# Optimization experiments

Hardware: AMD Instinct MI355X
Metric: run time of the kernel (lower is better)

## Reference

```python
import jax, jax.numpy as jnp
import numpy as np

B, N, DIM = 8, 1024, 768
HEADS, HEAD_DIM = 12, 64
INNER = HEADS * HEAD_DIM  # 768
SCALE = HEAD_DIM ** -0.5


def setup_inputs() -> dict:
    key = jax.random.key(0)
    k1, k2, k3, k4 = jax.random.split(key, 4)
    x = jax.random.normal(k1, (B, N, DIM), dtype=jnp.float32)
    # nn.Linear weights, stored as (in, out) for x @ W
    w_qkv = jax.random.normal(k2, (DIM, 3 * INNER), dtype=jnp.float32) * (DIM ** -0.5)
    w_out = jax.random.normal(k3, (INNER, DIM), dtype=jnp.float32) * (INNER ** -0.5)
    b_out = jax.random.normal(k4, (DIM,), dtype=jnp.float32) * 0.02
    return {"x": x, "w_qkv": w_qkv, "w_out": w_out, "b_out": b_out}


def reference(x, w_qkv, w_out, b_out):
    qkv = jnp.einsum('bnd,de->bne', x, w_qkv)  # [B, N, 3*INNER]
    q, k, v = jnp.split(qkv, 3, axis=-1)
    # 'b n (h d) -> b h n d'
    def split_heads(t):
        return t.reshape(B, N, HEADS, HEAD_DIM).transpose(0, 2, 1, 3)
    q, k, v = split_heads(q), split_heads(k), split_heads(v)
    score = jnp.einsum('bhnd,bhmd->bhnm', q, k) * SCALE  # [B, H, N, N]
    # Faithful to torch nn.Softmax() with dim=None on a 4D tensor: legacy
    # behavior applies softmax over dim=1 (the HEADS axis), NOT the key axis.
    attention = jax.nn.softmax(score, axis=1)
    out = jnp.einsum('bhnm,bhmd->bhnd', attention, v)  # [B, H, N, D]
    out = out.transpose(0, 2, 1, 3).reshape(B, N, INNER)  # 'b h n d -> b n (h d)'
    return jnp.einsum('bne,ed->bnd', out, w_out) + b_out
```

## Files before the change

### kernel.cpp

```cpp
#include <hip/hip_runtime.h>

typedef float  f32x4  __attribute__((ext_vector_type(4)));
typedef short  bf16x8 __attribute__((ext_vector_type(8)));

#define MFMA16(a, b, c) __builtin_amdgcn_mfma_f32_16x16x32_bf16((a), (b), (c), 0, 0, 0)

#define GLL16(g, l) __builtin_amdgcn_global_load_lds(                      \
    (const __attribute__((address_space(1))) void*)(g),                    \
    (__attribute__((address_space(3))) void*)(l), 16, 0, 0)

__device__ __forceinline__ short f2bf(float f) {
    union { float f; unsigned u; } a; a.f = f;
    unsigned r = a.u + 0x7fffu + ((a.u >> 16) & 1u);
    return (short)(r >> 16);
}
__device__ __forceinline__ float bf2f(unsigned short u) {
    union { unsigned u; float f; } a; a.u = ((unsigned)u) << 16; return a.f;
}

#define Bb   8
#define Nn   1024
#define DIM  768
#define HH   12
#define HD   64
#define INNER 768
#define SCALE 0.125f
#define SCL2E 0.18033688011112042f

__global__ void cast_to_bf16(const float* __restrict__ in, short* __restrict__ out, int n4) {
    int i = blockIdx.x * 256 + threadIdx.x;
    if (i >= n4) return;
    float4 f = reinterpret_cast<const float4*>(in)[i];
    unsigned lo = (unsigned)(unsigned short)f2bf(f.x) | ((unsigned)(unsigned short)f2bf(f.y) << 16);
    unsigned hi = (unsigned)(unsigned short)f2bf(f.z) | ((unsigned)(unsigned short)f2bf(f.w) << 16);
    reinterpret_cast<uint2*>(out)[i] = make_uint2(lo, hi);
}

__global__ __launch_bounds__(256, 8)
void transpose_cast_t(const float* __restrict__ w, short* __restrict__ wt,
                      int rows, int cols) {
    __shared__ float t[64][65];
    const int ntx = cols >> 6;
    const int bx = blockIdx.x % ntx;
    const int by = blockIdx.x / ntx;
    const int c0 = bx << 6, k0 = by << 6;
    const int tx = threadIdx.x & 63, ty = threadIdx.x >> 6;
#pragma unroll
    for (int j = 0; j < 64; j += 4)
        t[ty + j][tx] = w[(size_t)(k0 + ty + j) * cols + c0 + tx];
    __syncthreads();
#pragma unroll
    for (int j = 0; j < 64; j += 4)
        wt[(size_t)(c0 + ty + j) * rows + k0 + tx] = f2bf(t[tx][ty + j]);
}

#define STAGE(ksv, bv)                                                      \
  { const int kc_ = (ksv) << 5;                                             \
    GLL16(A  + aoff + kc_,                  &As[bv][lch]);                  \
    GLL16(A  + aoff + (size_t)64 * K + kc_, &As[bv][2048 + lch]);           \
    GLL16(Bt + boff + kc_,                  &Bs[bv][lch]);                  \
    GLL16(Bt + boff + (size_t)64 * K + kc_, &Bs[bv][2048 + lch]); }

#define PHASE(VM, DO_STAGE)                                                 \
  {                                                                         \
    bf16x8 af[4], bfr[4];                                                   \
    _Pragma("unroll") for (int t = 0; t < 4; t++)                           \
      af[t] = *reinterpret_cast<const bf16x8*>(                             \
          &As[bi][(wrow * 64 + t * 16 + l16) * 32 + swo]);                  \
    _Pragma("unroll") for (int t = 0; t < 4; t++)                           \
      bfr[t] = *reinterpret_cast<const bf16x8*>(                            \
          &Bs[bi][(wcol * 64 + t * 16 + l16) * 32 + swo]);                  \
    if (DO_STAGE) { STAGE(ks + 2, bn); }                                    \
    asm volatile("s_waitcnt vmcnt(" #VM ")" ::: "memory");                  \
    __builtin_amdgcn_s_barrier();                                           \
    asm volatile("s_waitcnt lgkmcnt(0)" ::: "memory");                      \
    __builtin_amdgcn_sched_barrier(0);                                      \
    __builtin_amdgcn_s_setprio(1);                                          \
    _Pragma("unroll") for (int rt = 0; rt < 4; rt++)                        \
      _Pragma("unroll") for (int ct = 0; ct < 4; ct++)                      \
        acc[rt][ct] = MFMA16(af[rt], bfr[ct], acc[rt][ct]);                 \
    __builtin_amdgcn_s_setprio(0);                                          \
    __builtin_amdgcn_s_barrier();                                           \
  }

template <int MODE>
__global__ __launch_bounds__(256, 3)
void gemm128(const short* __restrict__ A, const short* __restrict__ Bt, int K,
             short* __restrict__ qb, short* __restrict__ kb, short* __restrict__ vtb,
             float* __restrict__ outp, const float* __restrict__ bias) {
    __shared__ __align__(16) short As[3][128 * 32];
    __shared__ __align__(16) short Bs[3][128 * 32];

    const int tid  = threadIdx.x;
    const int lane = tid & 63, wv = tid >> 6;
    const int wrow = wv >> 1, wcol = wv & 1;
    const int quad = lane >> 4, l16 = lane & 15;

    const int bid = blockIdx.x;
    const int m0 = (((bid & 7) << 3) | ((bid >> 3) & 7)) << 7;
    const int n0 = (bid >> 6) << 7;

    const int row64 = (wv << 4) + (lane >> 2);
    const int gu = (lane & 3) ^ ((lane >> 3) & 3);
    const size_t aoff = (size_t)(m0 + row64) * K + gu * 8;
    const size_t boff = (size_t)(n0 + row64) * K + gu * 8;
    const int lch = wv * 512;

    f32x4 acc[4][4];
#pragma unroll
    for (int i = 0; i < 4; i++)
#pragma unroll
        for (int j = 0; j < 4; j++) acc[i][j] = (f32x4){0.f, 0.f, 0.f, 0.f};

    const int swo = (quad ^ ((l16 >> 1) & 3)) * 8;

    const int NK = K >> 5;

    STAGE(0, 0);
    STAGE(1, 1);
    asm volatile("s_waitcnt vmcnt(4)" ::: "memory");
    __builtin_amdgcn_s_barrier();

    int bi = 0, bn = 2;
    int ks = 0;
    for (; ks < NK - 2; ks++) {
        PHASE(4, true);
        bi = (bi == 2) ? 0 : bi + 1;
        bn = (bn == 2) ? 0 : bn + 1;
    }
    PHASE(0, false);
    bi = (bi == 2) ? 0 : bi + 1;
    PHASE(0, false);

#pragma unroll
    for (int rt = 0; rt < 4; rt++) {
#pragma unroll
        for (int ct = 0; ct < 4; ct++) {
            const int c = n0 + wcol * 64 + ct * 16 + l16;
#pragma unroll
            for (int reg = 0; reg < 4; reg++) {
                const int r = m0 + wrow * 64 + rt * 16 + quad * 4 + reg;
                const float v = acc[rt][ct][reg];
                if (MODE == 0) {
                    const int b = r >> 10, n = r & 1023;
                    const int which = (c >= 1536) ? 2 : (c >= 768 ? 1 : 0);
                    const int cc = c - which * 768;
                    const int h = cc >> 6, d = cc & 63;
                    const int bh = b * HH + h;
                    const short bv = f2bf(v);
                    if (which == 0)      qb[(bh << 16) + (n << 6) + d] = bv;
                    else if (which == 1) kb[(bh << 16) + (n << 6) + d] = bv;
                    else                 vtb[(bh << 16) + (d << 10) + n] = bv;
                } else {
                    outp[(size_t)r * 768 + c] = v + bias[c];
                }
            }
        }
    }
}

__global__ __launch_bounds__(512, 4)
void attn_den5(const short* __restrict__ qb, const short* __restrict__ kb,
               short* __restrict__ invp) {
    __shared__ __align__(16) short Qs[2][128 * 64];
    __shared__ __align__(16) short Ks[2][128 * 64];

    const int tid = threadIdx.x, lane = tid & 63, wv = tid >> 6;
    const int wrow = wv >> 2, wcol = wv & 3;
    const int quad = lane >> 4, l16 = lane & 15;
    const int bid = blockIdx.x;
    const int b = bid & 7;
    const int nmt = bid >> 3;
    const int n0 = (nmt >> 3) << 7;
    const int m0 = (nmt & 7) << 7;

    const int r8 = lane >> 3;
    const int gu = (lane & 7) ^ r8;
    const int qo0 = (n0 + wv * 8 + r8) * 64 + gu * 8;
    const int qo1 = qo0 + 64 * 64;
    const int ko0 = (m0 + wv * 8 + r8) * 64 + gu * 8;
    const int ko1 = ko0 + 64 * 64;
    const int lc0 = wv * 512;
    const int lc1 = 4096 + wv * 512;

    f32x4 den[4][2];
#pragma unroll
    for (int i = 0; i < 4; i++)
#pragma unroll
        for (int j = 0; j < 2; j++) den[i][j] = (f32x4){0.f, 0.f, 0.f, 0.f};
    const f32x4 z = (f32x4){0.f, 0.f, 0.f, 0.f};

    {
        const short* qh = qb + ((size_t)(b * HH) << 16);
        const short* kh = kb + ((size_t)(b * HH) << 16);
        GLL16(qh + qo0, &Qs[0][lc0]);
        GLL16(qh + qo1, &Qs[0][lc1]);
        GLL16(kh + ko0, &Ks[0][lc0]);
        GLL16(kh + ko1, &Ks[0][lc1]);
    }

    for (int h = 0; h < HH; h++) {
        asm volatile("s_waitcnt vmcnt(0)" ::: "memory");
        __syncthreads();
        if (h < HH - 1) {
            const int pn = (h + 1) & 1;
            const short* qh = qb + ((size_t)(b * HH + h + 1) << 16);
            const short* kh = kb + ((size_t)(b * HH + h + 1) << 16);
            GLL16(qh + qo0, &Qs[pn][lc0]);
            GLL16(qh + qo1, &Qs[pn][lc1]);
            GLL16(kh + ko0, &Ks[pn][lc0]);
            GLL16(kh + ko1, &Ks[pn][lc1]);
        }
        const int pb = h & 1;
        const int sw0 = (quad ^ (l16 & 7)) * 8;

        bf16x8 aq[4][2], bk[2][2];
#pragma unroll
        for (int t = 0; t < 4; t++) {
            const int row = wrow * 64 + t * 16 + l16;
            aq[t][0] = *reinterpret_cast<bf16x8*>(&Qs[pb][row * 64 + sw0]);
            aq[t][1] = *reinterpret_cast<bf16x8*>(&Qs[pb][row * 64 + (sw0 ^ 32)]);
        }
#pragma unroll
        for (int t = 0; t < 2; t++) {
            const int row = wcol * 32 + t * 16 + l16;
            bk[t][0] = *reinterpret_cast<bf16x8*>(&Ks[pb][row * 64 + sw0]);
            bk[t][1] = *reinterpret_cast<bf16x8*>(&Ks[pb][row * 64 + (sw0 ^ 32)]);
        }
#pragma unroll
        for (int nt = 0; nt < 4; nt++)
#pragma unroll
            for (int mt = 0; mt < 2; mt++) {
                f32x4 s = MFMA16(aq[nt][0], bk[mt][0], z);
                s = MFMA16(aq[nt][1], bk[mt][1], s);
#pragma unroll
                for (int r = 0; r < 4; r++)
                    den[nt][mt][r] += __builtin_amdgcn_exp2f(s[r] * SCL2E);
            }
    }

#pragma unroll
    for (int nt = 0; nt < 4; nt++)
#pragma unroll
        for (int mt = 0; mt < 2; mt++) {
            const int ntg = (n0 >> 4) + wrow * 4 + nt;
            const int mtg = (m0 >> 4) + wcol * 2 + mt;
            ushort4 o;
            o.x = (unsigned short)f2bf(1.0f / den[nt][mt][0]);
            o.y = (unsigned short)f2bf(1.0f / den[nt][mt][1]);
            o.z = (unsigned short)f2bf(1.0f / den[nt][mt][2]);
            o.w = (unsigned short)f2bf(1.0f / den[nt][mt][3]);
            *reinterpret_cast<ushort4*>(&invp[(((b * 64 + ntg) * 64 + mtg) * 64 + lane) * 4]) = o;
        }
}

__global__ __launch_bounds__(256, 4)
void attn_pv2(const short* __restrict__ qb, const short* __restrict__ kb,
              const short* __restrict__ vtb, const short* __restrict__ invp,
              short* __restrict__ attn_out) {
    __shared__ __align__(16) short Ks[2][32 * 72];
    __shared__ __align__(16) short Vs[2][64 * 40];
    __shared__ __align__(16) short Ps[4][32 * 40];

    const int tid = threadIdx.x, lane = tid & 63, wv = tid >> 6;
    const int quad = lane >> 4, l16 = lane & 15;
    const int bid = blockIdx.x;
    const int b = bid & 7;
    const int r = bid >> 3;
    const int n4 = r / 12;
    const int h = r - n4 * 12;
    const int nb = n4 << 7;
    const int bh = b * HH + h;

    bf16x8 aq[2][2];
#pragma unroll
    for (int nt = 0; nt < 2; nt++) {
        const short* qp = qb + (bh << 16) + ((nb + wv * 32 + nt * 16 + l16) << 6) + quad * 8;
        aq[nt][0] = *reinterpret_cast<const bf16x8*>(qp);
        aq[nt][1] = *reinterpret_cast<const bf16x8*>(qp + 32);
    }

    const f32x4 z = (f32x4){0.f, 0.f, 0.f, 0.f};
    f32x4 O[2][4];
#pragma unroll
    for (int nt = 0; nt < 2; nt++)
#pragma unroll
        for (int d = 0; d < 4; d++) O[nt][d] = z;

    const int krow = tid >> 3, koff = (tid & 7) * 8;
    const int vrow = tid >> 2, voff = (tid & 3) * 8;

    uint4 kreg = *reinterpret_cast<const uint4*>(kb + (bh << 16) + (krow << 6) + koff);
    uint4 vreg = *reinterpret_cast<const uint4*>(vtb + (bh << 16) + (vrow << 10) + voff);

    for (int it = 0; it < 32; it++) {
        const int p = it & 1;
        *reinterpret_cast<uint4*>(&Ks[p][krow * 72 + koff]) = kreg;
        *reinterpret_cast<uint4*>(&Vs[p][vrow * 40 + voff]) = vreg;
        __syncthreads();
        if (it < 31) {
            const int m1 = (it + 1) << 5;
            kreg = *reinterpret_cast<const uint4*>(kb + (bh << 16) + ((m1 + krow) << 6) + koff);
            vreg = *reinterpret_cast<const uint4*>(vtb + (bh << 16) + (vrow << 10) + m1 + voff);
        }
        const int m0 = it << 5;

#pragma unroll
        for (int mh = 0; mh < 2; mh++) {
            const bf16x8 k0 = *reinterpret_cast<bf16x8*>(&Ks[p][(mh * 16 + l16) * 72 + quad * 8]);
            const bf16x8 k1 = *reinterpret_cast<bf16x8*>(&Ks[p][(mh * 16 + l16) * 72 + quad * 8 + 32]);
            const int mt = (m0 >> 4) + mh;
#pragma unroll
            for (int nt = 0; nt < 2; nt++) {
                f32x4 s = MFMA16(aq[nt][0], k0, z);
                s = MFMA16(aq[nt][1], k1, s);
                const int ntg = (nb >> 4) + wv * 2 + nt;
                const ushort4 iv = *reinterpret_cast<const ushort4*>(
                    &invp[(((b * 64 + ntg) * 64 + mt) * 64 + lane) * 4]);
                Ps[wv][(nt * 16 + quad * 4 + 0) * 40 + mh * 16 + l16] = f2bf(__expf(s[0] * SCALE) * bf2f(iv.x));
                Ps[wv][(nt * 16 + quad * 4 + 1) * 40 + mh * 16 + l16] = f2bf(__expf(s[1] * SCALE) * bf2f(iv.y));
                Ps[wv][(nt * 16 + quad * 4 + 2) * 40 + mh * 16 + l16] = f2bf(__expf(s[2] * SCALE) * bf2f(iv.z));
                Ps[wv][(nt * 16 + quad * 4 + 3) * 40 + mh * 16 + l16] = f2bf(__expf(s[3] * SCALE) * bf2f(iv.w));
            }
        }
        __threadfence_block();

        bf16x8 pa[2];
#pragma unroll
        for (int nt = 0; nt < 2; nt++)
            pa[nt] = *reinterpret_cast<bf16x8*>(&Ps[wv][(nt * 16 + l16) * 40 + quad * 8]);
#pragma unroll
        for (int dch = 0; dch < 4; dch++) {
            const bf16x8 vf = *reinterpret_cast<bf16x8*>(&Vs[p][(dch * 16 + l16) * 40 + quad * 8]);
#pragma unroll
            for (int nt = 0; nt < 2; nt++)
                O[nt][dch] = MFMA16(pa[nt], vf, O[nt][dch]);
        }
    }

#pragma unroll
    for (int nt = 0; nt < 2; nt++)
#pragma unroll
        for (int dch = 0; dch < 4; dch++) {
            const int col = h * 64 + dch * 16 + l16;
#pragma unroll
            for (int reg = 0; reg < 4; reg++) {
                const int n = nb + wv * 32 + nt * 16 + quad * 4 + reg;
                attn_out[(size_t)((b << 10) + n) * 768 + col] = f2bf(O[nt][dch][reg]);
            }
        }
}

extern "C" void kernel_launch(void* const* d_in, const int* in_sizes, int n_in,
                              void* d_out, int out_size, void* d_ws, size_t ws_size,
                              hipStream_t stream) {
    const float* x     = (const float*)d_in[0];
    const float* w_qkv = (const float*)d_in[1];
    const float* w_out = (const float*)d_in[2];
    const float* b_out = (const float*)d_in[3];
    float* out = (float*)d_out;

    short* xb   = (short*)d_ws;
    short* wT1  = xb  + 8192 * 768;
    short* wT2  = wT1 + 2304 * 768;
    short* qb   = wT2 + 768 * 768;
    short* kb   = qb  + 96 * 65536;
    short* vtb  = kb  + 96 * 65536;
    short* attn = vtb + 96 * 65536;
    short* invp = attn + 8192 * 768;

    cast_to_bf16<<<6144, 256, 0, stream>>>(x, xb, (8192 * 768) / 4);
    transpose_cast_t<<<(768 / 64) * (2304 / 64), 256, 0, stream>>>(w_qkv, wT1, 768, 2304);
    transpose_cast_t<<<(768 / 64) * (768 / 64), 256, 0, stream>>>(w_out, wT2, 768, 768);

    gemm128<0><<<1152, 256, 0, stream>>>(
        xb, wT1, 768, qb, kb, vtb, nullptr, nullptr);

    attn_den5<<<512, 512, 0, stream>>>(qb, kb, invp);
    attn_pv2<<<768, 256, 0, stream>>>(qb, kb, vtb, invp, attn);

    gemm128<1><<<384, 256, 0, stream>>>(
        attn, wT2, 768, nullptr, nullptr, nullptr, out, b_out);
}
```

Before: 229.8 us.

## Fuse prep kernels into one launch and use 128x64 tiles for output GEMM

Folds the x cast and both weight transpose-casts into a single prep kernel that dispatches on block index, saving two launches. It also replaces the output projection's 128x128 GEMM (384 blocks) with a dedicated 128x64-tile kernel launched as 768 blocks, using a three-buffer LDS pipeline and grouped block ordering. The aim is to fill the GPU's CUs better on the small final GEMM, at the cost of reloading the A tiles more often.

```diff
diff --git a/kernel.cpp b/kernel.cpp
--- a/kernel.cpp
+++ b/kernel.cpp
@@ -27,22 +27,27 @@
 #define SCALE 0.125f
 #define SCL2E 0.18033688011112042f
 
-__global__ void cast_to_bf16(const float* __restrict__ in, short* __restrict__ out, int n4) {
-    int i = blockIdx.x * 256 + threadIdx.x;
-    if (i >= n4) return;
-    float4 f = reinterpret_cast<const float4*>(in)[i];
-    unsigned lo = (unsigned)(unsigned short)f2bf(f.x) | ((unsigned)(unsigned short)f2bf(f.y) << 16);
-    unsigned hi = (unsigned)(unsigned short)f2bf(f.z) | ((unsigned)(unsigned short)f2bf(f.w) << 16);
-    reinterpret_cast<uint2*>(out)[i] = make_uint2(lo, hi);
-}
-
 __global__ __launch_bounds__(256, 8)
-void transpose_cast_t(const float* __restrict__ w, short* __restrict__ wt,
-                      int rows, int cols) {
+void prep(const float* __restrict__ x, short* __restrict__ xb,
+          const float* __restrict__ w_qkv, short* __restrict__ wT1,
+          const float* __restrict__ w_out, short* __restrict__ wT2) {
     __shared__ float t[64][65];
+    const int bid = blockIdx.x;
+    if (bid < 6144) {
+        const int i = bid * 256 + threadIdx.x;
+        float4 f = reinterpret_cast<const float4*>(x)[i];
+        unsigned lo = (unsigned)(unsigned short)f2bf(f.x) | ((unsigned)(unsigned short)f2bf(f.y) << 16);
+        unsigned hi = (unsigned)(unsigned short)f2bf(f.z) | ((unsigned)(unsigned short)f2bf(f.w) << 16);
+        reinterpret_cast<uint2*>(xb)[i] = make_uint2(lo, hi);
+        return;
+    }
+    const float* w; short* wt; int cols, tix;
+    if (bid < 6576) { w = w_qkv; wt = wT1; cols = 2304; tix = bid - 6144; }
+    else            { w = w_out; wt = wT2; cols = 768;  tix = bid - 6576; }
+    const int rows = 768;
     const int ntx = cols >> 6;
-    const int bx = blockIdx.x % ntx;
-    const int by = blockIdx.x / ntx;
+    const int bx = tix % ntx;
+    const int by = tix / ntx;
     const int c0 = bx << 6, k0 = by << 6;
     const int tx = threadIdx.x & 63, ty = threadIdx.x >> 6;
 #pragma unroll
@@ -159,6 +164,95 @@
     }
 }
 
+#define OSTAGE(ksv, bv)                                                     \
+  { const int kc_ = (ksv) << 5;                                             \
+    GLL16(A  + aoff + kc_,                  &As[bv][lch]);                  \
+    GLL16(A  + aoff + (size_t)64 * K + kc_, &As[bv][2048 + lch]);           \
+    GLL16(Bt + boff + kc_,                  &Bs[bv][lch]); }
+
+#define OPHASE(VM, DO_STAGE)                                                \
+  {                                                                         \
+    bf16x8 af[4], bfr[2];                                                   \
+    _Pragma("unroll") for (int t = 0; t < 4; t++)                           \
+      af[t] = *reinterpret_cast<const bf16x8*>(                             \
+          &As[bi][(wrow * 64 + t * 16 + l16) * 32 + swo]);                  \
+    _Pragma("unroll") for (int t = 0; t < 2; t++)                           \
+      bfr[t] = *reinterpret_cast<const bf16x8*>(                            \
+          &Bs[bi][(wcol * 32 + t * 16 + l16) * 32 + swo]);                  \
+    if (DO_STAGE) { OSTAGE(ks + 2, bn); }                                   \
+    asm volatile("s_waitcnt vmcnt(" #VM ")" ::: "memory");                  \
+    __builtin_amdgcn_s_barrier();                                           \
+    asm volatile("s_waitcnt lgkmcnt(0)" ::: "memory");                      \
+    __builtin_amdgcn_sched_barrier(0);                                      \
+    __builtin_amdgcn_s_setprio(1);                                          \
+    _Pragma("unroll") for (int rt = 0; rt < 4; rt++)                        \
+      _Pragma("unroll") for (int ct = 0; ct < 2; ct++)                      \
+        acc[rt][ct] = MFMA16(af[rt], bfr[ct], acc[rt][ct]);                 \
+    __builtin_amdgcn_s_setprio(0);                                          \
+    __builtin_amdgcn_s_barrier();                                           \
+  }
+
+__global__ __launch_bounds__(256, 4)
+void gemm_o(const short* __restrict__ A, const short* __restrict__ Bt, int K,
+            float* __restrict__ outp, const float* __restrict__ bias) {
+    __shared__ __align__(16) short As[3][128 * 32];
+    __shared__ __align__(16) short Bs[3][64 * 32];
+
+    const int tid  = threadIdx.x;
+    const int lane = tid & 63, wv = tid >> 6;
+    const int wrow = wv >> 1, wcol = wv & 1;
+    const int quad = lane >> 4, l16 = lane & 15;
+
+    const int bid = blockIdx.x;
+    const int m0 = (((bid & 7) << 3) | ((bid >> 3) & 7)) << 7;
+    const int n0 = (bid >> 6) << 6;
+
+    const int row64 = (wv << 4) + (lane >> 2);
+    const int gu = (lane & 3) ^ ((lane >> 3) & 3);
+    const size_t aoff = (size_t)(m0 + row64) * K + gu * 8;
+    const size_t boff = (size_t)(n0 + row64) * K + gu * 8;
+    const int lch = wv * 512;
+
+    f32x4 acc[4][2];
+#pragma unroll
+    for (int i = 0; i < 4; i++)
+#pragma unroll
+        for (int j = 0; j < 2; j++) acc[i][j] = (f32x4){0.f, 0.f, 0.f, 0.f};
+
+    const int swo = (quad ^ ((l16 >> 1) & 3)) * 8;
+
+    const int NK = K >> 5;
+
+    OSTAGE(0, 0);
+    OSTAGE(1, 1);
+    asm volatile("s_waitcnt vmcnt(3)" ::: "memory");
+    __builtin_amdgcn_s_barrier();
+
+    int bi = 0, bn = 2;
+    int ks = 0;
+    for (; ks < NK - 2; ks++) {
+        OPHASE(3, true);
+        bi = (bi == 2) ? 0 : bi + 1;
+        bn = (bn == 2) ? 0 : bn + 1;
+    }
+    OPHASE(0, false);
+    bi = (bi == 2) ? 0 : bi + 1;
+    OPHASE(0, false);
+
+#pragma unroll
+    for (int rt = 0; rt < 4; rt++) {
+#pragma unroll
+        for (int ct = 0; ct < 2; ct++) {
+            const int c = n0 + wcol * 32 + ct * 16 + l16;
+#pragma unroll
+            for (int reg = 0; reg < 4; reg++) {
+                const int r = m0 + wrow * 64 + rt * 16 + quad * 4 + reg;
+                outp[(size_t)r * 768 + c] = acc[rt][ct][reg] + bias[c];
+            }
+        }
+    }
+}
+
 __global__ __launch_bounds__(512, 4)
 void attn_den5(const short* __restrict__ qb, const short* __restrict__ kb,
                short* __restrict__ invp) {
@@ -369,9 +463,7 @@
     short* attn = vtb + 96 * 65536;
     short* invp = attn + 8192 * 768;
 
-    cast_to_bf16<<<6144, 256, 0, stream>>>(x, xb, (8192 * 768) / 4);
-    transpose_cast_t<<<(768 / 64) * (2304 / 64), 256, 0, stream>>>(w_qkv, wT1, 768, 2304);
-    transpose_cast_t<<<(768 / 64) * (768 / 64), 256, 0, stream>>>(w_out, wT2, 768, 768);
+    prep<<<6720, 256, 0, stream>>>(x, xb, w_qkv, wT1, w_out, wT2);
 
     gemm128<0><<<1152, 256, 0, stream>>>(
         xb, wT1, 768, qb, kb, vtb, nullptr, nullptr);
@@ -379,6 +471,5 @@
     attn_den5<<<512, 512, 0, stream>>>(qb, kb, invp);
     attn_pv2<<<768, 256, 0, stream>>>(qb, kb, vtb, invp, attn);
 
-    gemm128<1><<<384, 256, 0, stream>>>(
-        attn, wT2, 768, nullptr, nullptr, nullptr, out, b_out);
-}
+    gemm_o<<<768, 256, 0, stream>>>(attn, wT2, 768, out, b_out);
+}
```

New measurement: 224.3 us. 1.02x faster.
